# Performance work log

Measured on AMD Instinct MI355X. Metric: run time of the kernel, lower is better.

Reference implementation:

```python
import jax, jax.numpy as jnp
import numpy as np

B, N, L = 1, 256, 512
D_MSA, D_PAIR, H, D = 256, 128, 8, 32
SCALING = 1.0 / float(np.sqrt(D))
EPS = 1e-5


def layer_norm(x, g, b):
    mu = jnp.mean(x, axis=-1, keepdims=True)
    var = jnp.mean(jnp.square(x - mu), axis=-1, keepdims=True)
    return (x - mu) * jax.lax.rsqrt(var + EPS) * g + b


def setup_inputs() -> dict:
    key = jax.random.key(0)
    ks = jax.random.split(key, 16)
    inp = {
        "msa": jax.random.normal(ks[0], (B, N, L, D_MSA), dtype=jnp.float32),
        "pair": jax.random.normal(ks[1], (B, L, L, D_PAIR), dtype=jnp.float32),
        "ln_msa_g": 1.0 + 0.1 * jax.random.normal(ks[2], (D_MSA,), dtype=jnp.float32),
        "ln_msa_b": 0.1 * jax.random.normal(ks[3], (D_MSA,), dtype=jnp.float32),
        "ln_pair_g": 1.0 + 0.1 * jax.random.normal(ks[4], (D_PAIR,), dtype=jnp.float32),
        "ln_pair_b": 0.1 * jax.random.normal(ks[5], (D_PAIR,), dtype=jnp.float32),
        "w_q": 0.02 * jax.random.normal(ks[6], (D_MSA, H * D), dtype=jnp.float32),
        "w_k": 0.02 * jax.random.normal(ks[7], (D_MSA, H * D), dtype=jnp.float32),
        "w_v": 0.02 * jax.random.normal(ks[8], (D_MSA, H * D), dtype=jnp.float32),
        "w_b": 0.02 * jax.random.normal(ks[9], (D_PAIR, H), dtype=jnp.float32),
        "w_g": 0.02 * jax.random.normal(ks[10], (D_MSA, H * D), dtype=jnp.float32),
        "b_g": jnp.ones((H * D,), dtype=jnp.float32),
        "w_out": 0.02 * jax.random.normal(ks[11], (H * D, D_MSA), dtype=jnp.float32),
        "b_out": jnp.zeros((D_MSA,), dtype=jnp.float32),
        "mask": jax.random.randint(ks[12], (B, L), 0, 2, dtype=jnp.int32),
    }
    return inp


def reference(msa, pair, ln_msa_g, ln_msa_b, ln_pair_g, ln_pair_b,
              w_q, w_k, w_v, w_b, w_g, b_g, w_out, b_out, mask):
    # mask == 0 means padded/invalid position (torch: mask = mask == 0)
    pad = (mask == 0)  # [B, L] bool
    msa = jnp.nan_to_num(msa)
    pair = jnp.nan_to_num(pair)
    msa_n = layer_norm(msa, ln_msa_g, ln_msa_b)          # [B,N,L,d_msa]
    pair_n = layer_norm(pair, ln_pair_g, ln_pair_b)       # [B,L,L,d_pair]

    q = (msa_n @ w_q).reshape(B, N, L, H, D)
    k = (msa_n @ w_k).reshape(B, N, L, H, D)
    v = (msa_n @ w_v).reshape(B, N, L, H, D)
    bias = pair_n @ w_b                                    # [B,L,L,H]
    gate = jax.nn.sigmoid(msa_n @ w_g + b_g)               # [B,N,L,H*D]

    fill = pad[:, None, :, None, None]                     # [B,1,L,1,1]
    zero = jnp.zeros((), dtype=q.dtype)
    q = jnp.where(fill, zero, q)
    v = jnp.where(fill, zero, v)
    k = jnp.where(fill, zero, k) * jnp.asarray(SCALING, dtype=k.dtype)

    # reduce over both MSA-sequence dim n and head dim d
    attn = jnp.einsum('bnqhd,bnkhd->bqkh', q, k) + bias    # [B,L,L,H]
    mask2d = pad[:, :, None] | pad[:, None, :]             # [B,L,L]
    attn = jnp.where(mask2d[..., None], jnp.asarray(-1e9, attn.dtype), attn)
    attn = jax.nn.softmax(attn, axis=2)                    # softmax over k

    out = jnp.einsum('bqkh,bnkhd->bnqhd', attn, v).reshape(B, N, L, H * D)
    out = gate * out
    out = out @ w_out + b_out                              # [B,N,L,d_msa]
    out = jnp.where(pad[:, None, :, None], jnp.zeros((), out.dtype), out)
    return out
```

## Files before the change

### kernel.cpp

```cpp
#include <hip/hip_runtime.h>
#include <hip/hip_bf16.h>
#include <math.h>

typedef __bf16 bf16_t;
typedef float f32x4 __attribute__((ext_vector_type(4)));
typedef __bf16 bf16x8 __attribute__((ext_vector_type(8)));
typedef __bf16 bf16x4 __attribute__((ext_vector_type(4)));
typedef int i32x4 __attribute__((ext_vector_type(4)));

#define SCALING 0.17677669529663687f
#define LNEPS 1e-5f

#define OFF_QKG   0u
#define OFF_LOG   201326592u
#define OFF_BIAS  209715200u
#define OFF_P     218103808u
#define OFF_WT    222298112u
#define OFF_WTO   222822400u
#define OFF_FLAG  222953472u

#define GLOBAL_AS __attribute__((address_space(1)))
#define LDS_AS    __attribute__((address_space(3)))

static __device__ __forceinline__ f32x4 mfma16(bf16x8 a, bf16x8 b, f32x4 c) {
  return __builtin_amdgcn_mfma_f32_16x16x32_bf16(a, b, c, 0, 0, 0);
}

static __device__ __forceinline__ float ldf(const void* p, int i, int is32) {
  return is32 ? ((const float*)p)[i] : (float)((const bf16_t*)p)[i];
}
static __device__ __forceinline__ float scrubf(float x) {
  if (x != x) return 0.f;
  return fminf(fmaxf(x, -3.3e38f), 3.3e38f);
}

__global__ __launch_bounds__(256) void k_detect(const unsigned short* raw, int* flag) {
  __shared__ int s;
  int t = threadIdx.x;
  if (t == 0) s = 0;
  __syncthreads();
  int local = 0;
  for (int i = 0; i < 16; i++) {
    unsigned short u = raw[t * 16 + i];
    int e = (u >> 7) & 0xFF;
    if (e >= 170) local = 1;
  }
  if (local) s = 1;
  __syncthreads();
  if (t == 0) *flag = s;
}

__global__ __launch_bounds__(256) void k_transpose(
    const void* wq, const void* wk, const void* wv, const void* wg,
    const void* wout, const int* flag, bf16_t* wt_cat, bf16_t* wt_out) {
  int is32 = *flag;
  int idx = blockIdx.x * 256 + threadIdx.x;
  if (idx < 1024 * 256) {
    int c = idx >> 8, k = idx & 255;
    const void* src = (c < 256) ? wq : (c < 512) ? wk : (c < 768) ? wv : wg;
    wt_cat[c * 256 + (k ^ ((c & 7) << 3))] = (bf16_t)ldf(src, k * 256 + (c & 255), is32);
  } else {
    int i2 = idx - 1024 * 256;
    int c = i2 >> 8, k = i2 & 255;
    wt_out[c * 256 + k] = (bf16_t)ldf(wout, k * 256 + c, is32);
  }
}

__global__ __launch_bounds__(256) void k_pair_bias(
    const void* pair, const void* g, const void* b,
    const void* wb, const int* flag, float* bias_ws) {
  __shared__ float wbs[128 * 8];
  __shared__ float gs[128], bs[128];
  int is32 = *flag;
  int t = threadIdx.x;
  if (t < 128) { gs[t] = ldf(g, t, is32); bs[t] = ldf(b, t, is32); }
  for (int i = t; i < 1024; i += 256) wbs[i] = ldf(wb, i, is32);
  __syncthreads();
  int lane = t & 63, w = t >> 6;
  int j = lane & 7;
  int rowg = lane >> 3;
  float gr[16], br[16];
#pragma unroll
  for (int e = 0; e < 16; e++) { gr[e] = gs[j * 16 + e]; br[e] = bs[j * 16 + e]; }
  int row0 = blockIdx.x * 64 + w * 16;
#pragma unroll
  for (int pass = 0; pass < 2; pass++) {
    int row = row0 + pass * 8 + rowg;
    float x[16];
    if (is32) {
#pragma unroll
      for (int i = 0; i < 4; i++) {
        f32x4 v = *(const f32x4*)((const float*)pair + (size_t)row * 128 + j * 16 + i * 4);
#pragma unroll
        for (int e = 0; e < 4; e++) x[i * 4 + e] = scrubf(v[e]);
      }
    } else {
#pragma unroll
      for (int i = 0; i < 2; i++) {
        i32x4 raw = *(const i32x4*)((const bf16_t*)pair + (size_t)row * 128 + j * 16 + i * 8);
        const bf16_t* sp = (const bf16_t*)&raw;
#pragma unroll
        for (int e = 0; e < 8; e++) x[i * 8 + e] = scrubf((float)sp[e]);
      }
    }
    float s = 0.f, sq = 0.f;
#pragma unroll
    for (int e = 0; e < 16; e++) { s += x[e]; sq += x[e] * x[e]; }
#pragma unroll
    for (int o = 1; o <= 4; o <<= 1) {
      s += __shfl_xor(s, o, 64);
      sq += __shfl_xor(sq, o, 64);
    }
    float mu = s * (1.f / 128.f);
    float var = sq * (1.f / 128.f) - mu * mu;
    float rs = rsqrtf(fmaxf(var, 0.f) + LNEPS);
    float ph[8] = {0.f, 0.f, 0.f, 0.f, 0.f, 0.f, 0.f, 0.f};
#pragma unroll
    for (int e = 0; e < 16; e++) {
      float xn = (x[e] - mu) * rs * gr[e] + br[e];
      const float* wp = wbs + (j * 16 + e) * 8;
      f32x4 w0 = *(const f32x4*)wp;
      f32x4 w1 = *(const f32x4*)(wp + 4);
#pragma unroll
      for (int hh = 0; hh < 4; hh++) { ph[hh] += xn * w0[hh]; ph[4 + hh] += xn * w1[hh]; }
    }
#pragma unroll
    for (int o = 1; o <= 4; o <<= 1) {
#pragma unroll
      for (int hh = 0; hh < 8; hh++) ph[hh] += __shfl_xor(ph[hh], o, 64);
    }
    if (j == 0) {
      int qp = row >> 9, kp = row & 511;
      float* bp = bias_ws + (size_t)qp * 512 + kp;
#pragma unroll
      for (int hh = 0; hh < 8; hh++) bp[(size_t)hh * 262144] = ph[hh];
    }
  }
}

static __device__ __forceinline__ void issue_b(const bf16_t* wtc, int col0, int half,
                                               char* dst, int t) {
#pragma unroll
  for (int j = 0; j < 4; ++j) {
    int o = t * 16 + j * 8192;
    int row = o >> 8, within = o & 255;
    const char* src = (const char*)wtc + (size_t)(col0 + row) * 512 + half * 256 + within;
    __builtin_amdgcn_global_load_lds((const GLOBAL_AS void*)src,
                                     (LDS_AS void*)(dst + o), 16, 0, 0);
  }
}

__global__ __launch_bounds__(512) void k_proj(
    const void* msa, const void* lng, const void* lnb,
    const bf16_t* wt_cat, const void* bg, const int* mask, const int* flag,
    bf16_t* qkg, bf16_t* vt) {
  __shared__ __align__(16) char lds[100352];
  bf16_t* As = (bf16_t*)lds;
  char* buf0 = lds + 67584;
  char* buf1 = lds;
  int is32 = *flag;
  int t = threadIdx.x, lane = t & 63, w = t >> 6;
  int wr = w & 1, wc = w >> 1;
  int hi = lane >> 4, cl = lane & 15;
  int row0 = blockIdx.x * 128;

  {
    int ar = t >> 2;
    int ac = (t & 3) << 6;
    float xv[64];
    if (is32) {
      const float* xr = (const float*)msa + (size_t)(row0 + ar) * 256 + ac;
#pragma unroll
      for (int i = 0; i < 16; ++i) {
        f32x4 v = *(const f32x4*)(xr + i * 4);
#pragma unroll
        for (int e = 0; e < 4; ++e) xv[i * 4 + e] = scrubf(v[e]);
      }
    } else {
      const bf16_t* xr = (const bf16_t*)msa + (size_t)(row0 + ar) * 256 + ac;
#pragma unroll
      for (int i = 0; i < 8; ++i) {
        i32x4 raw = *(const i32x4*)(xr + i * 8);
        const bf16_t* sp = (const bf16_t*)&raw;
#pragma unroll
        for (int e = 0; e < 8; ++e) xv[i * 8 + e] = scrubf((float)sp[e]);
      }
    }
    float s = 0.f, sq = 0.f;
#pragma unroll
    for (int i = 0; i < 64; ++i) { s += xv[i]; sq += xv[i] * xv[i]; }
    s += __shfl_xor(s, 1, 64); sq += __shfl_xor(sq, 1, 64);
    s += __shfl_xor(s, 2, 64); sq += __shfl_xor(sq, 2, 64);
    float mu = s * (1.f / 256.f);
    float var = sq * (1.f / 256.f) - mu * mu;
    float rs = rsqrtf(fmaxf(var, 0.f) + LNEPS);
    if (is32) {
      const float* gp = (const float*)lng + ac;
      const float* bp = (const float*)lnb + ac;
#pragma unroll
      for (int i = 0; i < 16; ++i) {
        f32x4 g = *(const f32x4*)(gp + i * 4);
        f32x4 b = *(const f32x4*)(bp + i * 4);
        bf16x4 y;
#pragma unroll
        for (int e = 0; e < 4; ++e)
          y[e] = (bf16_t)((xv[i * 4 + e] - mu) * rs * g[e] + b[e]);
        *(bf16x4*)(As + (size_t)ar * 264 + ac + i * 4) = y;
      }
    } else {
      const bf16_t* gp = (const bf16_t*)lng + ac;
      const bf16_t* bp = (const bf16_t*)lnb + ac;
#pragma unroll
      for (int i = 0; i < 8; ++i) {
        i32x4 gr = *(const i32x4*)(gp + i * 8);
        i32x4 br = *(const i32x4*)(bp + i * 8);
        const bf16_t* gs = (const bf16_t*)&gr;
        const bf16_t* bs = (const bf16_t*)&br;
        bf16x8 y;
#pragma unroll
        for (int e = 0; e < 8; ++e)
          y[e] = (bf16_t)((xv[i * 8 + e] - mu) * rs * (float)gs[e] + (float)bs[e]);
        *(bf16x8*)(As + (size_t)ar * 264 + ac + i * 8) = y;
      }
    }
  }
  __syncthreads();
  issue_b(wt_cat, 0, 0, buf0, t);

  bf16x8 aall[8][4];
  {
    int arow = wr * 64 + cl;
#pragma unroll
    for (int ks = 0; ks < 8; ++ks)
#pragma unroll
      for (int m = 0; m < 4; ++m)
        aall[ks][m] = *(const bf16x8*)(As + (size_t)(arow + m * 16) * 264 + ks * 32 + hi * 8);
  }
  __syncthreads();

  int brow0 = wc * 32 + cl, brow1 = brow0 + 16;
  int rbase = row0 + wr * 64 + hi * 4;
  unsigned padbits = 0;
#pragma unroll
  for (int m = 0; m < 4; ++m)
#pragma unroll
    for (int i = 0; i < 4; ++i)
      if (mask[(rbase + m * 16 + i) & 511] == 0) padbits |= 1u << (m * 4 + i);

  f32x4 z = {0.f, 0.f, 0.f, 0.f};
  f32x4 acc[4][2] = {{z, z}, {z, z}, {z, z}, {z, z}};

  for (int bn = 0; bn < 8; ++bn) {
    issue_b(wt_cat, bn << 7, 1, buf1, t);
#pragma unroll
    for (int kk = 0; kk < 4; ++kk) {
      int k8 = kk * 4 + hi;
      bf16x8 b0 = *(const bf16x8*)(buf0 + brow0 * 256 + ((k8 ^ (brow0 & 7)) << 4));
      bf16x8 b1 = *(const bf16x8*)(buf0 + brow1 * 256 + ((k8 ^ (brow1 & 7)) << 4));
#pragma unroll
      for (int m = 0; m < 4; ++m) {
        acc[m][0] = mfma16(aall[kk][m], b0, acc[m][0]);
        acc[m][1] = mfma16(aall[kk][m], b1, acc[m][1]);
      }
    }
    __syncthreads();
    if (bn < 7) issue_b(wt_cat, (bn + 1) << 7, 0, buf0, t);
#pragma unroll
    for (int kk = 0; kk < 4; ++kk) {
      int k8 = kk * 4 + hi;
      bf16x8 b0 = *(const bf16x8*)(buf1 + brow0 * 256 + ((k8 ^ (brow0 & 7)) << 4));
      bf16x8 b1 = *(const bf16x8*)(buf1 + brow1 * 256 + ((k8 ^ (brow1 & 7)) << 4));
#pragma unroll
      for (int m = 0; m < 4; ++m) {
        acc[m][0] = mfma16(aall[4 + kk][m], b0, acc[m][0]);
        acc[m][1] = mfma16(aall[4 + kk][m], b1, acc[m][1]);
      }
    }
    __syncthreads();
    int region = bn >> 1;
    int col0 = bn << 7;
#pragma unroll
    for (int m = 0; m < 4; ++m) {
#pragma unroll
      for (int n = 0; n < 2; ++n) {
        int col = col0 + wc * 32 + n * 16 + cl;
#pragma unroll
        for (int i = 0; i < 4; ++i) {
          int r = rbase + m * 16 + i;
          bool pad = (padbits >> (m * 4 + i)) & 1;
          float v = acc[m][n][i];
          if (region == 0) {
            qkg[(size_t)r * 768 + col] = (bf16_t)(pad ? 0.f : v);
          } else if (region == 1) {
            qkg[(size_t)r * 768 + col] = (bf16_t)(pad ? 0.f : v * SCALING);
          } else if (region == 2) {
            int hd = col & 255;
            vt[((size_t)((r >> 9) * 8 + (hd >> 5)) * 32 + (hd & 31)) * 512 + (r & 511)] =
                (bf16_t)(pad ? 0.f : v);
          } else {
            int gcol = col & 255;
            float xg = v + ldf(bg, gcol, is32);
            qkg[(size_t)r * 768 + 512 + gcol] = (bf16_t)(1.f / (1.f + __expf(-xg)));
          }
          acc[m][n][i] = 0.f;
        }
      }
    }
  }
}

__global__ __launch_bounds__(256) void k_logits(const bf16_t* qkg, float* logit_ws) {
  __shared__ bf16_t As[64 * 136];
  __shared__ bf16_t Bs[64 * 136];
  int t = threadIdx.x, lane = t & 63, w = t >> 6;
  int j = blockIdx.x;
  int jj = (j & 7) * 64 + (j >> 3);
  int ktile = jj & 7, qtile = (jj >> 3) & 7, h = jj >> 6;
  int mw = w & 1, nw = w >> 1;
  f32x4 z = {0.f, 0.f, 0.f, 0.f};
  f32x4 acc[2][2] = {{z, z}, {z, z}};
  for (int s = 0; s < 64; s++) {
    int kk0 = s * 128;
#pragma unroll
    for (int i = 0; i < 4; i++) {
      int flat = t + i * 256;
      int r = flat >> 4, c8 = flat & 15;
      int kk = kk0 + c8 * 8;
      int n = kk >> 5, d = kk & 31;
      i32x4 va = *(const i32x4*)(qkg + ((size_t)(n * 512 + qtile * 64 + r)) * 768 + h * 32 + d);
      *(i32x4*)(As + r * 136 + c8 * 8) = va;
      i32x4 vb = *(const i32x4*)(qkg + ((size_t)(n * 512 + ktile * 64 + r)) * 768 + 256 + h * 32 + d);
      *(i32x4*)(Bs + r * 136 + c8 * 8) = vb;
    }
    __syncthreads();
#pragma unroll
    for (int kk = 0; kk < 128; kk += 32) {
      int ko = kk + (lane >> 4) * 8;
      bf16x8 a0 = *(const bf16x8*)(As + (mw * 32 + (lane & 15)) * 136 + ko);
      bf16x8 a1 = *(const bf16x8*)(As + (mw * 32 + 16 + (lane & 15)) * 136 + ko);
      bf16x8 b0 = *(const bf16x8*)(Bs + (nw * 32 + (lane & 15)) * 136 + ko);
      bf16x8 b1 = *(const bf16x8*)(Bs + (nw * 32 + 16 + (lane & 15)) * 136 + ko);
      acc[0][0] = mfma16(a0, b0, acc[0][0]);
      acc[0][1] = mfma16(a0, b1, acc[0][1]);
      acc[1][0] = mfma16(a1, b0, acc[1][0]);
      acc[1][1] = mfma16(a1, b1, acc[1][1]);
    }
    __syncthreads();
  }
  int quad = lane >> 4, cl = lane & 15;
#pragma unroll
  for (int mt = 0; mt < 2; mt++) {
#pragma unroll
    for (int nt = 0; nt < 2; nt++) {
      int kp = ktile * 64 + nw * 32 + nt * 16 + cl;
#pragma unroll
      for (int i = 0; i < 4; i++) {
        int q = qtile * 64 + mw * 32 + mt * 16 + quad * 4 + i;
        logit_ws[((size_t)(h * 512 + q)) * 512 + kp] = acc[mt][nt][i];
      }
    }
  }
}

__global__ __launch_bounds__(256) void k_softmax(
    const float* logit_ws, const float* bias_ws, const int* mask, bf16_t* p_ws) {
  __shared__ float red[8];
  int t = threadIdx.x;
  int hq = blockIdx.x;
  int q = hq & 511;
  bool padq = (mask[q] == 0);
  const float* lg = logit_ws + (size_t)hq * 512;
  const float* bi = bias_ws + (size_t)(hq >> 9) * 262144 + (size_t)q * 512;
  int k0 = t * 2;
  float v0 = lg[k0] + bi[k0];
  float v1 = lg[k0 + 1] + bi[k0 + 1];
  if (padq || mask[k0] == 0) v0 = -1e9f;
  if (padq || mask[k0 + 1] == 0) v1 = -1e9f;
  float m = fmaxf(v0, v1);
#pragma unroll
  for (int o = 32; o >= 1; o >>= 1) m = fmaxf(m, __shfl_xor(m, o, 64));
  if ((t & 63) == 0) red[t >> 6] = m;
  __syncthreads();
  m = fmaxf(fmaxf(red[0], red[1]), fmaxf(red[2], red[3]));
  float e0 = __expf(v0 - m), e1 = __expf(v1 - m);
  float s = e0 + e1;
#pragma unroll
  for (int o = 32; o >= 1; o >>= 1) s += __shfl_xor(s, o, 64);
  if ((t & 63) == 0) red[4 + (t >> 6)] = s;
  __syncthreads();
  s = red[4] + red[5] + red[6] + red[7];
  float inv = 1.f / s;
  p_ws[(size_t)hq * 512 + k0] = (bf16_t)(e0 * inv);
  p_ws[(size_t)hq * 512 + k0 + 1] = (bf16_t)(e1 * inv);
}

__global__ __launch_bounds__(256) void k_av(
    const bf16_t* p_ws, const bf16_t* vt, bf16_t* qkg) {
  __shared__ bf16_t Ps[64 * 136];
  __shared__ bf16_t Vs[32 * 136];
  int t = threadIdx.x, lane = t & 63, w = t >> 6;
  int j = blockIdx.x;
  int jj = (j & 7) * 2048 + (j >> 3);
  int qt = jj & 7;
  int n = (jj >> 3) & 255;
  int h = jj >> 11;
  f32x4 z = {0.f, 0.f, 0.f, 0.f};
  f32x4 acc[2] = {z, z};
  for (int s = 0; s < 4; s++) {
    int k0 = s * 128;
#pragma unroll
    for (int i = 0; i < 4; i++) {
      int flat = t + i * 256;
      int r = flat >> 4, c8 = flat & 15;
      *(i32x4*)(Ps + r * 136 + c8 * 8) =
          *(const i32x4*)(p_ws + ((size_t)(h * 512 + qt * 64 + r)) * 512 + k0 + c8 * 8);
    }
#pragma unroll
    for (int i = 0; i < 2; i++) {
      int flat = t + i * 256;
      int r = flat >> 4, c8 = flat & 15;
      *(i32x4*)(Vs + r * 136 + c8 * 8) =
          *(const i32x4*)(vt + ((size_t)((n * 8 + h) * 32 + r)) * 512 + k0 + c8 * 8);
    }
    __syncthreads();
#pragma unroll
    for (int kk = 0; kk < 128; kk += 32) {
      int ko = kk + (lane >> 4) * 8;
      bf16x8 a = *(const bf16x8*)(Ps + (w * 16 + (lane & 15)) * 136 + ko);
      bf16x8 b0 = *(const bf16x8*)(Vs + ((lane & 15)) * 136 + ko);
      bf16x8 b1 = *(const bf16x8*)(Vs + (16 + (lane & 15)) * 136 + ko);
      acc[0] = mfma16(a, b0, acc[0]);
      acc[1] = mfma16(a, b1, acc[1]);
    }
    __syncthreads();
  }
  int quad = lane >> 4, cl = lane & 15;
#pragma unroll
  for (int nt = 0; nt < 2; nt++) {
#pragma unroll
    for (int i = 0; i < 4; i++) {
      int q = qt * 64 + w * 16 + quad * 4 + i;
      int d = nt * 16 + cl;
      size_t base = ((size_t)(n * 512 + q)) * 768;
      float gate = (float)qkg[base + 512 + h * 32 + d];
      qkg[base + h * 32 + d] = (bf16_t)(acc[nt][i] * gate);
    }
  }
}

__global__ __launch_bounds__(256) void k_out(
    const bf16_t* qkg, const bf16_t* wt_out, const void* b_out,
    const int* mask, const int* flag, void* outp) {
  __shared__ bf16_t As[64 * 72];
  __shared__ bf16_t Bs[64 * 72];
  int is32 = *flag;
  int t = threadIdx.x, lane = t & 63, w = t >> 6;
  int bm = blockIdx.x >> 2, bn = blockIdx.x & 3;
  int row0 = bm * 64;
  int mw = w & 1, nw = w >> 1;
  f32x4 z = {0.f, 0.f, 0.f, 0.f};
  f32x4 acc[2][2] = {{z, z}, {z, z}};
  for (int kt = 0; kt < 4; kt++) {
#pragma unroll
    for (int i = 0; i < 2; i++) {
      int flat = t + i * 256;
      int r = flat >> 3, c8 = flat & 7;
      *(i32x4*)(As + r * 72 + c8 * 8) =
          *(const i32x4*)(qkg + (size_t)(row0 + r) * 768 + kt * 64 + c8 * 8);
      *(i32x4*)(Bs + r * 72 + c8 * 8) =
          *(const i32x4*)(wt_out + (size_t)(bn * 64 + r) * 256 + kt * 64 + c8 * 8);
    }
    __syncthreads();
#pragma unroll
    for (int kk = 0; kk < 64; kk += 32) {
      int ko = kk + (lane >> 4) * 8;
      bf16x8 a0 = *(const bf16x8*)(As + (mw * 32 + (lane & 15)) * 72 + ko);
      bf16x8 a1 = *(const bf16x8*)(As + (mw * 32 + 16 + (lane & 15)) * 72 + ko);
      bf16x8 b0 = *(const bf16x8*)(Bs + (nw * 32 + (lane & 15)) * 72 + ko);
      bf16x8 b1 = *(const bf16x8*)(Bs + (nw * 32 + 16 + (lane & 15)) * 72 + ko);
      acc[0][0] = mfma16(a0, b0, acc[0][0]);
      acc[0][1] = mfma16(a0, b1, acc[0][1]);
      acc[1][0] = mfma16(a1, b0, acc[1][0]);
      acc[1][1] = mfma16(a1, b1, acc[1][1]);
    }
    __syncthreads();
  }
  int quad = lane >> 4, cl = lane & 15;
#pragma unroll
  for (int mt = 0; mt < 2; mt++) {
#pragma unroll
    for (int nt = 0; nt < 2; nt++) {
      int col = bn * 64 + nw * 32 + nt * 16 + cl;
      float bo = ldf(b_out, col, is32);
#pragma unroll
      for (int i = 0; i < 4; i++) {
        int r = row0 + mw * 32 + mt * 16 + quad * 4 + i;
        int l = r & 511;
        float v = acc[mt][nt][i] + bo;
        if (mask[l] == 0) v = 0.f;
        if (is32) ((float*)outp)[(size_t)r * 256 + col] = v;
        else ((bf16_t*)outp)[(size_t)r * 256 + col] = (bf16_t)v;
      }
    }
  }
}

extern "C" void kernel_launch(void* const* d_in, const int* in_sizes, int n_in,
                              void* d_out, int out_size, void* d_ws, size_t ws_size,
                              hipStream_t stream) {
  const void* msa      = d_in[0];
  const void* pair     = d_in[1];
  const void* ln_msa_g = d_in[2];
  const void* ln_msa_b = d_in[3];
  const void* ln_pair_g= d_in[4];
  const void* ln_pair_b= d_in[5];
  const void* w_q      = d_in[6];
  const void* w_k      = d_in[7];
  const void* w_v      = d_in[8];
  const void* w_b      = d_in[9];
  const void* w_g      = d_in[10];
  const void* b_g      = d_in[11];
  const void* w_out    = d_in[12];
  const void* b_out    = d_in[13];
  const int*  mask     = (const int*)d_in[14];

  char* ws = (char*)d_ws;
  bf16_t* qkg   = (bf16_t*)(ws + OFF_QKG);
  float*  logit = (float*)(ws + OFF_LOG);
  float*  biasb = (float*)(ws + OFF_BIAS);
  bf16_t* pbuf  = (bf16_t*)(ws + OFF_P);
  bf16_t* wtc   = (bf16_t*)(ws + OFF_WT);
  bf16_t* wto   = (bf16_t*)(ws + OFF_WTO);
  int*    flag  = (int*)(ws + OFF_FLAG);
  bf16_t* vt    = (bf16_t*)d_out;

  k_detect<<<1, 256, 0, stream>>>((const unsigned short*)msa, flag);
  k_transpose<<<1280, 256, 0, stream>>>(w_q, w_k, w_v, w_g, w_out, flag, wtc, wto);
  k_pair_bias<<<4096, 256, 0, stream>>>(pair, ln_pair_g, ln_pair_b, w_b, flag, biasb);
  k_proj<<<1024, 512, 0, stream>>>(msa, ln_msa_g, ln_msa_b, wtc, b_g, mask, flag, qkg, vt);
  k_logits<<<512, 256, 0, stream>>>(qkg, logit);
  k_softmax<<<4096, 256, 0, stream>>>(logit, biasb, mask, pbuf);
  k_av<<<16384, 256, 0, stream>>>(pbuf, vt, qkg);
  k_out<<<8192, 256, 0, stream>>>(qkg, wto, b_out, mask, flag, d_out);
}
```

Measured before the change: 853.9 us.

## Split MSA layernorm into its own kernel and triple-buffer weight loads in projection

Moves the MSA layernorm out of the projection kernel into a separate k_ln kernel. It writes swizzled bf16 normalized rows into the gate slot of the qkg workspace, which the projection later overwrites. The projection kernel then loads its A tile with async global-to-LDS copies and streams weight half-tiles through a three-buffer rotation, using explicit vmcnt waits instead of two full syncthreads per step. The gate bias is hoisted into registers. The aim is to overlap weight loads with MFMA work and cut register and LDS pressure in k_proj, at the cost of an extra kernel launch and an extra round trip of the normalized activations through global memory.

```diff
diff --git a/kernel.cpp b/kernel.cpp
--- a/kernel.cpp
+++ b/kernel.cpp
@@ -63,6 +63,45 @@
     int i2 = idx - 1024 * 256;
     int c = i2 >> 8, k = i2 & 255;
     wt_out[c * 256 + k] = (bf16_t)ldf(wout, k * 256 + c, is32);
+  }
+}
+
+__global__ __launch_bounds__(256) void k_ln(
+    const void* msa, const void* g, const void* b, const int* flag, bf16_t* qkg) {
+  int is32 = *flag;
+  int t = threadIdx.x, lane = t & 63, w = t >> 6;
+  int c0 = lane * 4;
+  float gv[4], bv[4];
+#pragma unroll
+  for (int e = 0; e < 4; e++) { gv[e] = ldf(g, c0 + e, is32); bv[e] = ldf(b, c0 + e, is32); }
+  int row0 = blockIdx.x * 64 + w * 16;
+  for (int rr = 0; rr < 16; rr++) {
+    int r = row0 + rr;
+    float x[4];
+    if (is32) {
+      f32x4 v = *(const f32x4*)((const float*)msa + (size_t)r * 256 + c0);
+#pragma unroll
+      for (int e = 0; e < 4; e++) x[e] = scrubf(v[e]);
+    } else {
+      bf16x4 v = *(const bf16x4*)((const bf16_t*)msa + (size_t)r * 256 + c0);
+#pragma unroll
+      for (int e = 0; e < 4; e++) x[e] = scrubf((float)v[e]);
+    }
+    float s = x[0] + x[1] + x[2] + x[3];
+    float sq = x[0] * x[0] + x[1] * x[1] + x[2] * x[2] + x[3] * x[3];
+#pragma unroll
+    for (int o = 32; o >= 1; o >>= 1) {
+      s += __shfl_xor(s, o, 64);
+      sq += __shfl_xor(sq, o, 64);
+    }
+    float mu = s * (1.f / 256.f);
+    float var = sq * (1.f / 256.f) - mu * mu;
+    float rs = rsqrtf(fmaxf(var, 0.f) + LNEPS);
+    bf16x4 y;
+#pragma unroll
+    for (int e = 0; e < 4; e++) y[e] = (bf16_t)((x[e] - mu) * rs * gv[e] + bv[e]);
+    int pc = (lane >> 1) ^ (r & 7);
+    *(bf16x4*)((char*)qkg + ((size_t)r * 768 + 512) * 2 + pc * 16 + (lane & 1) * 8) = y;
   }
 }
 
@@ -151,134 +190,69 @@
 }
 
 __global__ __launch_bounds__(512) void k_proj(
-    const void* msa, const void* lng, const void* lnb,
     const bf16_t* wt_cat, const void* bg, const int* mask, const int* flag,
     bf16_t* qkg, bf16_t* vt) {
-  __shared__ __align__(16) char lds[100352];
-  bf16_t* As = (bf16_t*)lds;
-  char* buf0 = lds + 67584;
-  char* buf1 = lds;
+  __shared__ __align__(16) char lds[98304];
+  char* B0 = lds + 65536;
+  char* B1 = lds;
+  char* B2 = lds + 32768;
   int is32 = *flag;
   int t = threadIdx.x, lane = t & 63, w = t >> 6;
   int wr = w & 1, wc = w >> 1;
   int hi = lane >> 4, cl = lane & 15;
   int row0 = blockIdx.x * 128;
-
-  {
-    int ar = t >> 2;
-    int ac = (t & 3) << 6;
-    float xv[64];
-    if (is32) {
-      const float* xr = (const float*)msa + (size_t)(row0 + ar) * 256 + ac;
-#pragma unroll
-      for (int i = 0; i < 16; ++i) {
-        f32x4 v = *(const f32x4*)(xr + i * 4);
-#pragma unroll
-        for (int e = 0; e < 4; ++e) xv[i * 4 + e] = scrubf(v[e]);
-      }
-    } else {
-      const bf16_t* xr = (const bf16_t*)msa + (size_t)(row0 + ar) * 256 + ac;
-#pragma unroll
-      for (int i = 0; i < 8; ++i) {
-        i32x4 raw = *(const i32x4*)(xr + i * 8);
-        const bf16_t* sp = (const bf16_t*)&raw;
-#pragma unroll
-        for (int e = 0; e < 8; ++e) xv[i * 8 + e] = scrubf((float)sp[e]);
-      }
-    }
-    float s = 0.f, sq = 0.f;
-#pragma unroll
-    for (int i = 0; i < 64; ++i) { s += xv[i]; sq += xv[i] * xv[i]; }
-    s += __shfl_xor(s, 1, 64); sq += __shfl_xor(sq, 1, 64);
-    s += __shfl_xor(s, 2, 64); sq += __shfl_xor(sq, 2, 64);
-    float mu = s * (1.f / 256.f);
-    float var = sq * (1.f / 256.f) - mu * mu;
-    float rs = rsqrtf(fmaxf(var, 0.f) + LNEPS);
-    if (is32) {
-      const float* gp = (const float*)lng + ac;
-      const float* bp = (const float*)lnb + ac;
-#pragma unroll
-      for (int i = 0; i < 16; ++i) {
-        f32x4 g = *(const f32x4*)(gp + i * 4);
-        f32x4 b = *(const f32x4*)(bp + i * 4);
-        bf16x4 y;
-#pragma unroll
-        for (int e = 0; e < 4; ++e)
-          y[e] = (bf16_t)((xv[i * 4 + e] - mu) * rs * g[e] + b[e]);
-        *(bf16x4*)(As + (size_t)ar * 264 + ac + i * 4) = y;
-      }
-    } else {
-      const bf16_t* gp = (const bf16_t*)lng + ac;
-      const bf16_t* bp = (const bf16_t*)lnb + ac;
-#pragma unroll
-      for (int i = 0; i < 8; ++i) {
-        i32x4 gr = *(const i32x4*)(gp + i * 8);
-        i32x4 br = *(const i32x4*)(bp + i * 8);
-        const bf16_t* gs = (const bf16_t*)&gr;
-        const bf16_t* bs = (const bf16_t*)&br;
-        bf16x8 y;
-#pragma unroll
-        for (int e = 0; e < 8; ++e)
-          y[e] = (bf16_t)((xv[i * 8 + e] - mu) * rs * (float)gs[e] + (float)bs[e]);
-        *(bf16x8*)(As + (size_t)ar * 264 + ac + i * 8) = y;
-      }
-    }
-  }
-  __syncthreads();
-  issue_b(wt_cat, 0, 0, buf0, t);
+  int rbase = row0 + wr * 64 + hi * 4;
+
+  unsigned padbits = 0;
+#pragma unroll
+  for (int m = 0; m < 4; ++m)
+#pragma unroll
+    for (int i = 0; i < 4; ++i)
+      if (mask[(rbase + m * 16 + i) & 511] == 0) padbits |= 1u << (m * 4 + i);
+  float bgv[2][2];
+#pragma unroll
+  for (int bb = 0; bb < 2; ++bb)
+#pragma unroll
+    for (int n = 0; n < 2; ++n)
+      bgv[bb][n] = ldf(bg, bb * 128 + wc * 32 + n * 16 + cl, is32);
+
+#pragma unroll
+  for (int j = 0; j < 8; ++j) {
+    int o = t * 16 + j * 8192;
+    int row = o >> 9, within = o & 511;
+    const char* src = (const char*)qkg + ((size_t)(row0 + row) * 768 + 512) * 2 + within;
+    __builtin_amdgcn_global_load_lds((const GLOBAL_AS void*)src,
+                                     (LDS_AS void*)(lds + o), 16, 0, 0);
+  }
+  issue_b(wt_cat, 0, 0, B0, t);
+  asm volatile("s_waitcnt vmcnt(4)" ::: "memory");
+  __builtin_amdgcn_s_barrier();
+  asm volatile("" ::: "memory");
 
   bf16x8 aall[8][4];
   {
     int arow = wr * 64 + cl;
+    int sw = (cl & 7) << 4;
 #pragma unroll
     for (int ks = 0; ks < 8; ++ks)
 #pragma unroll
       for (int m = 0; m < 4; ++m)
-        aall[ks][m] = *(const bf16x8*)(As + (size_t)(arow + m * 16) * 264 + ks * 32 + hi * 8);
-  }
-  __syncthreads();
+        aall[ks][m] = *(const bf16x8*)(lds + (size_t)(arow + m * 16) * 512 +
+                                       (((ks * 4 + hi) << 4) ^ sw));
+  }
+  asm volatile("s_waitcnt lgkmcnt(0)" ::: "memory");
+  __builtin_amdgcn_sched_barrier(0);
+  __builtin_amdgcn_s_barrier();
+  asm volatile("" ::: "memory");
+  issue_b(wt_cat, 0, 1, B1, t);
 
   int brow0 = wc * 32 + cl, brow1 = brow0 + 16;
-  int rbase = row0 + wr * 64 + hi * 4;
-  unsigned padbits = 0;
-#pragma unroll
-  for (int m = 0; m < 4; ++m)
-#pragma unroll
-    for (int i = 0; i < 4; ++i)
-      if (mask[(rbase + m * 16 + i) & 511] == 0) padbits |= 1u << (m * 4 + i);
-
+  int sb = (brow0 & 7) << 4;
   f32x4 z = {0.f, 0.f, 0.f, 0.f};
   f32x4 acc[4][2] = {{z, z}, {z, z}, {z, z}, {z, z}};
 
-  for (int bn = 0; bn < 8; ++bn) {
-    issue_b(wt_cat, bn << 7, 1, buf1, t);
-#pragma unroll
-    for (int kk = 0; kk < 4; ++kk) {
-      int k8 = kk * 4 + hi;
-      bf16x8 b0 = *(const bf16x8*)(buf0 + brow0 * 256 + ((k8 ^ (brow0 & 7)) << 4));
-      bf16x8 b1 = *(const bf16x8*)(buf0 + brow1 * 256 + ((k8 ^ (brow1 & 7)) << 4));
-#pragma unroll
-      for (int m = 0; m < 4; ++m) {
-        acc[m][0] = mfma16(aall[kk][m], b0, acc[m][0]);
-        acc[m][1] = mfma16(aall[kk][m], b1, acc[m][1]);
-      }
-    }
-    __syncthreads();
-    if (bn < 7) issue_b(wt_cat, (bn + 1) << 7, 0, buf0, t);
-#pragma unroll
-    for (int kk = 0; kk < 4; ++kk) {
-      int k8 = kk * 4 + hi;
-      bf16x8 b0 = *(const bf16x8*)(buf1 + brow0 * 256 + ((k8 ^ (brow0 & 7)) << 4));
-      bf16x8 b1 = *(const bf16x8*)(buf1 + brow1 * 256 + ((k8 ^ (brow1 & 7)) << 4));
-#pragma unroll
-      for (int m = 0; m < 4; ++m) {
-        acc[m][0] = mfma16(aall[4 + kk][m], b0, acc[m][0]);
-        acc[m][1] = mfma16(aall[4 + kk][m], b1, acc[m][1]);
-      }
-    }
-    __syncthreads();
-    int region = bn >> 1;
-    int col0 = bn << 7;
+  auto epilogue = [&](int bn) {
+    int region = bn >> 1, col0 = bn << 7;
 #pragma unroll
     for (int m = 0; m < 4; ++m) {
 #pragma unroll
@@ -298,15 +272,54 @@
             vt[((size_t)((r >> 9) * 8 + (hd >> 5)) * 32 + (hd & 31)) * 512 + (r & 511)] =
                 (bf16_t)(pad ? 0.f : v);
           } else {
-            int gcol = col & 255;
-            float xg = v + ldf(bg, gcol, is32);
-            qkg[(size_t)r * 768 + 512 + gcol] = (bf16_t)(1.f / (1.f + __expf(-xg)));
+            float xg = v + bgv[bn & 1][n];
+            qkg[(size_t)r * 768 + 512 + (col & 255)] = (bf16_t)(1.f / (1.f + __expf(-xg)));
           }
           acc[m][n][i] = 0.f;
         }
       }
     }
-  }
+  };
+
+#define PROJ_STEP(I, RB, WB, CNT) do {                                         \
+    asm volatile("s_waitcnt vmcnt(" #CNT ")" ::: "memory");                    \
+    __builtin_amdgcn_s_barrier();                                              \
+    asm volatile("" ::: "memory");                                             \
+    if ((I) < 14) issue_b(wt_cat, (((I) + 2) >> 1) << 7, ((I) + 2) & 1, WB, t);\
+    {                                                                          \
+      const char* rb = (RB);                                                   \
+      _Pragma("unroll")                                                        \
+      for (int kk = 0; kk < 4; ++kk) {                                         \
+        int k8 = (kk * 4 + hi) << 4;                                           \
+        bf16x8 b0 = *(const bf16x8*)(rb + brow0 * 256 + (k8 ^ sb));            \
+        bf16x8 b1 = *(const bf16x8*)(rb + brow1 * 256 + (k8 ^ sb));            \
+        _Pragma("unroll")                                                      \
+        for (int m = 0; m < 4; ++m) {                                          \
+          acc[m][0] = mfma16(aall[((I) & 1) * 4 + kk][m], b0, acc[m][0]);      \
+          acc[m][1] = mfma16(aall[((I) & 1) * 4 + kk][m], b1, acc[m][1]);      \
+        }                                                                      \
+      }                                                                        \
+    }                                                                          \
+    if ((I) & 1) epilogue((I) >> 1);                                           \
+  } while (0)
+
+  PROJ_STEP(0,  B0, B2, 4);
+  PROJ_STEP(1,  B1, B0, 4);
+  PROJ_STEP(2,  B2, B1, 36);
+  PROJ_STEP(3,  B0, B2, 36);
+  PROJ_STEP(4,  B1, B0, 36);
+  PROJ_STEP(5,  B2, B1, 36);
+  PROJ_STEP(6,  B0, B2, 36);
+  PROJ_STEP(7,  B1, B0, 36);
+  PROJ_STEP(8,  B2, B1, 36);
+  PROJ_STEP(9,  B0, B2, 36);
+  PROJ_STEP(10, B1, B0, 36);
+  PROJ_STEP(11, B2, B1, 36);
+  PROJ_STEP(12, B0, B2, 36);
+  PROJ_STEP(13, B1, B0, 36);
+  PROJ_STEP(14, B2, B1, 36);
+  PROJ_STEP(15, B0, B2, 36);
+#undef PROJ_STEP
 }
 
 __global__ __launch_bounds__(256) void k_logits(const bf16_t* qkg, float* logit_ws) {
@@ -536,8 +549,9 @@
 
   k_detect<<<1, 256, 0, stream>>>((const unsigned short*)msa, flag);
   k_transpose<<<1280, 256, 0, stream>>>(w_q, w_k, w_v, w_g, w_out, flag, wtc, wto);
+  k_ln<<<2048, 256, 0, stream>>>(msa, ln_msa_g, ln_msa_b, flag, qkg);
   k_pair_bias<<<4096, 256, 0, stream>>>(pair, ln_pair_g, ln_pair_b, w_b, flag, biasb);
-  k_proj<<<1024, 512, 0, stream>>>(msa, ln_msa_g, ln_msa_b, wtc, b_g, mask, flag, qkg, vt);
+  k_proj<<<1024, 512, 0, stream>>>(wtc, b_g, mask, flag, qkg, vt);
   k_logits<<<512, 256, 0, stream>>>(qkg, logit);
   k_softmax<<<4096, 256, 0, stream>>>(logit, biasb, mask, pbuf);
   k_av<<<16384, 256, 0, stream>>>(pbuf, vt, qkg);
```

Measured after the change: 992.9 us. 1.16x slower.
